# Kernel tuning notes

Hardware: AMD Instinct MI355X
Metric: run time of the kernel (lower is better)

The kernel has to match this reference:

```python
import jax, jax.numpy as jnp
import numpy as np

B, T, E, H, V = 64, 512, 256, 512, 32000  # batch, n_step, emb_size=input_size, hidden_size, n_class


def setup_inputs() -> dict:
    key = jax.random.key(0)
    ks = jax.random.split(key, 32)
    stdv = 1.0 / np.sqrt(H)  # init_weights: uniform(-1/sqrt(hidden), +1/sqrt(hidden)) on ALL params
    u = lambda k, shape: jax.random.uniform(k, shape, jnp.float32, -stdv, stdv)
    X = jax.random.randint(ks[0], (B, T), 0, V, dtype=jnp.int64)
    inp = {
        "X": X,
        "emb": u(ks[1], (V, E)),
        # layer 0 gates (U_c/V_c/b_c, V_o, b_o are dead in forward -> omitted)
        "U_f": u(ks[2], (E, H)), "V_f": u(ks[3], (H, H)), "b_f": u(ks[4], (H,)),
        "U_i": u(ks[5], (E, H)), "V_i": u(ks[6], (H, H)), "b_i": u(ks[7], (H,)),
        "U_g": u(ks[8], (E, H)), "V_g": u(ks[9], (H, H)), "b_g": u(ks[10], (H,)),
        "U_o": u(ks[11], (E, H)),
        # layer 1 gates (U_c1/V_c1/b_c1 dead -> omitted)
        "U_f1": u(ks[12], (H, H)), "V_f1": u(ks[13], (H, H)), "b_f1": u(ks[14], (H,)),
        "U_i1": u(ks[15], (H, H)), "V_i1": u(ks[16], (H, H)), "b_i1": u(ks[17], (H,)),
        "U_g1": u(ks[18], (H, H)), "V_g1": u(ks[19], (H, H)), "b_g1": u(ks[20], (H,)),
        "U_o1": u(ks[21], (H, H)), "V_o1": u(ks[22], (H, H)), "b_o1": u(ks[23], (H,)),
        # output head: nn.Linear(H, n_class, bias=False) -> store as [H, V]; b starts as ones then re-init uniform
        "W_out": u(ks[24], (H, V)), "b_out": u(ks[25], (V,)),
    }
    return inp


def reference(X, emb, U_f, V_f, b_f, U_i, V_i, b_i, U_g, V_g, b_g, U_o,
              U_f1, V_f1, b_f1, U_i1, V_i1, b_i1, U_g1, V_g1, b_g1,
              U_o1, V_o1, b_o1, W_out, b_out):
    x = emb[X]                      # [B, T, E]
    xs = jnp.swapaxes(x, 0, 1)      # [T, B, E] for scan over time

    def step(carry, x_t):
        h, c, h1, c1 = carry
        # layer 0 (NOTE: original code uses V_o1 and b_o1 for layer-0 output gate)
        f = jax.nn.sigmoid(x_t @ U_f + h @ V_f + b_f)
        i = jax.nn.sigmoid(x_t @ U_i + h @ V_i + b_i)
        g = jnp.tanh(x_t @ U_g + h @ V_g + b_g)
        c = f * c + i * g
        o = jax.nn.sigmoid(x_t @ U_o + h @ V_o1 + b_o1)
        h = o * jnp.tanh(c)
        # layer 1
        f1 = jax.nn.sigmoid(h @ U_f1 + h1 @ V_f1 + b_f1)
        i1 = jax.nn.sigmoid(h @ U_i1 + h1 @ V_i1 + b_i1)
        g1 = jnp.tanh(h @ U_g1 + h1 @ V_g1 + b_g1)
        c1 = f1 * c1 + i1 * g1
        o1 = jax.nn.sigmoid(h @ U_o1 + h1 @ V_o1 + b_o1)
        h1 = o1 * jnp.tanh(c1)
        return (h, c, h1, c1), None

    ones = jnp.ones((B, H), jnp.float32)  # original inits states to ONES
    (h, c, h1, c1), _ = jax.lax.scan(step, (ones, ones, ones, ones), xs)
    # original: model = self.U(outputs) + self.U(outputs) + self.b  (U applied twice, V unused)
    proj = h1 @ W_out
    return proj + proj + b_out      # [B, V]
```

## Files before the change

kernel.cpp:

```cpp
#include <hip/hip_runtime.h>
#include <hip/hip_bf16.h>

typedef __attribute__((ext_vector_type(8))) short bf16x8;
typedef __attribute__((ext_vector_type(4))) float f32x4;
typedef __attribute__((ext_vector_type(2))) int int32x2;

constexpr int kB = 64;
constexpr int kT = 512;
constexpr int kE = 256;
constexpr int kH = 512;
constexpr int kV = 32000;
constexpr int kBH = kB * kH;
constexpr int FSTR = 16;

static __device__ __forceinline__ unsigned short f2bf(float x) {
  __hip_bfloat16 h = __float2bfloat16(x);
  return __builtin_bit_cast(unsigned short, h);
}

static __device__ __forceinline__ f32x4 mfma16(bf16x8 a, bf16x8 b, f32x4 c) {
  return __builtin_amdgcn_mfma_f32_16x16x32_bf16(a, b, c, 0, 0, 0);
}

static __device__ __forceinline__ void issue16_sc1(const unsigned short* p, bf16x8* a) {
  asm volatile(
      "global_load_dwordx4 %0, %16, off sc1\n\t"
      "global_load_dwordx4 %1, %16, off offset:64 sc1\n\t"
      "global_load_dwordx4 %2, %16, off offset:128 sc1\n\t"
      "global_load_dwordx4 %3, %16, off offset:192 sc1\n\t"
      "global_load_dwordx4 %4, %16, off offset:256 sc1\n\t"
      "global_load_dwordx4 %5, %16, off offset:320 sc1\n\t"
      "global_load_dwordx4 %6, %16, off offset:384 sc1\n\t"
      "global_load_dwordx4 %7, %16, off offset:448 sc1\n\t"
      "global_load_dwordx4 %8, %16, off offset:512 sc1\n\t"
      "global_load_dwordx4 %9, %16, off offset:576 sc1\n\t"
      "global_load_dwordx4 %10, %16, off offset:640 sc1\n\t"
      "global_load_dwordx4 %11, %16, off offset:704 sc1\n\t"
      "global_load_dwordx4 %12, %16, off offset:768 sc1\n\t"
      "global_load_dwordx4 %13, %16, off offset:832 sc1\n\t"
      "global_load_dwordx4 %14, %16, off offset:896 sc1\n\t"
      "global_load_dwordx4 %15, %16, off offset:960 sc1"
      : "=&v"(a[0]), "=&v"(a[1]), "=&v"(a[2]), "=&v"(a[3]),
        "=&v"(a[4]), "=&v"(a[5]), "=&v"(a[6]), "=&v"(a[7]),
        "=&v"(a[8]), "=&v"(a[9]), "=&v"(a[10]), "=&v"(a[11]),
        "=&v"(a[12]), "=&v"(a[13]), "=&v"(a[14]), "=&v"(a[15])
      : "v"(p));
}

static __device__ __forceinline__ void wait_frags16(bf16x8* a) {
  asm volatile("s_waitcnt vmcnt(0)"
               : "+v"(a[0]), "+v"(a[1]), "+v"(a[2]), "+v"(a[3]),
                 "+v"(a[4]), "+v"(a[5]), "+v"(a[6]), "+v"(a[7]),
                 "+v"(a[8]), "+v"(a[9]), "+v"(a[10]), "+v"(a[11]),
                 "+v"(a[12]), "+v"(a[13]), "+v"(a[14]), "+v"(a[15])
               :
               : "memory");
}

static __device__ __forceinline__ void store_dwordx2_sc1(unsigned short* p, int32x2 v) {
  asm volatile("global_store_dwordx2 %0, %1, off sc1" ::"v"(p), "v"(v) : "memory");
}

static __device__ __forceinline__ void store_int_sc1(int* p, int v) {
  asm volatile("global_store_dword %0, %1, off sc1" ::"v"(p), "v"(v) : "memory");
}

static __device__ __forceinline__ void pollgate(const int* p, int thr) {
  while (true) {
    int v;
    asm volatile("global_load_dword %0, %1, off sc1\n\ts_waitcnt vmcnt(0)"
                 : "=&v"(v)
                 : "v"(p)
                 : "memory");
    if (__all(v >= thr)) break;
  }
}

__global__ void pack_w(const float* __restrict__ s0, const float* __restrict__ s1,
                       const float* __restrict__ s2, const float* __restrict__ s3,
                       unsigned short* __restrict__ dst, int K) {
  int o = blockIdx.x * 256 + threadIdx.x;
  if (o >= K * 2048) return;
  int j = o & 7;
  int lane = (o >> 3) & 63;
  int gate = (o >> 9) & 3;
  int r2 = o >> 11;
  int kc = r2 % (K / 32);
  int hb = r2 / (K / 32);
  int k = kc * 32 + (lane >> 4) * 8 + j;
  int hid = hb * 16 + (lane & 15);
  const float* s = (gate == 0) ? s0 : (gate == 1) ? s1 : (gate == 2) ? s2 : s3;
  dst[o] = f2bf(s[(size_t)k * kH + hid]);
}

__global__ void gather_x(const int* __restrict__ X, const float* __restrict__ emb,
                         unsigned short* __restrict__ xseq) {
  int o = blockIdx.x * 256 + threadIdx.x;
  if (o >= kT * kB * (kE / 8)) return;
  int e8 = o & 31;
  int b = (o >> 5) & 63;
  int t = o >> 11;
  int tok = X[b * kT + t];
  const float* src = emb + (size_t)tok * kE + e8 * 8;
  unsigned short tmp[8];
#pragma unroll
  for (int j = 0; j < 8; ++j) tmp[j] = f2bf(src[j]);
  unsigned short* dst = xseq + ((size_t)t * kB + b) * kE + e8 * 8;
#pragma unroll
  for (int j = 0; j < 8; ++j) dst[j] = tmp[j];
}

__global__ void init_state(unsigned short* hbuf, unsigned short* h1buf,
                           float* bcat0, float* bcat1, int* fl0, int* fl1,
                           const float* b_f, const float* b_i, const float* b_g,
                           const float* b_o1,
                           const float* b_f1, const float* b_i1, const float* b_g1) {
  int i = blockIdx.x * 256 + threadIdx.x;
  if (i < 8 * kBH) hbuf[i] = 0x3F80u;
  if (i < 2 * kBH) h1buf[i] = 0x3F80u;
  if (i < 512) {
    bcat0[i] = b_f[i];  bcat0[512 + i] = b_i[i];
    bcat0[1024 + i] = b_g[i];  bcat0[1536 + i] = b_o1[i];
    bcat1[i] = b_f1[i]; bcat1[512 + i] = b_i1[i];
    bcat1[1024 + i] = b_g1[i]; bcat1[1536 + i] = b_o1[i];
  }
  if (i < 4 * 32 * FSTR) { fl0[i] = 0; fl1[i] = 0; }
}

__global__ void __launch_bounds__(64, 1)
lstm_rec(const unsigned short* __restrict__ xseq,
         const unsigned short* __restrict__ U0p, const unsigned short* __restrict__ V0p,
         const unsigned short* __restrict__ U1p, const unsigned short* __restrict__ V1p,
         const float* __restrict__ bcat0, const float* __restrict__ bcat1,
         unsigned short* __restrict__ hbuf,
         unsigned short* __restrict__ h1buf,
         float* __restrict__ h1f,
         int* __restrict__ fl0,
         int* __restrict__ fl1)
{
  extern __shared__ unsigned short lds[];
  const int lane = threadIdx.x;
  const int wg = blockIdx.x;
  const bool isL1 = wg >= 128;
  const int wl = wg & 127;
  const int hb = wl >> 2, bt = wl & 3;
  const int l15 = lane & 15, g4 = lane >> 4;
  const int batch = bt * 16 + l15;
  const int hid4 = hb * 16 + g4 * 4;
  const int KU = isL1 ? 512 : 256;

  {
    const unsigned short* Wu = isL1 ? U1p : U0p;
    const unsigned short* Wv = isL1 ? V1p : V0p;
    const int nu = KU * 64, nv = 512 * 64;
    const bf16x8* su = (const bf16x8*)(Wu + (size_t)hb * nu);
    bf16x8* d = (bf16x8*)lds;
    for (int i = lane; i < nu / 8; i += 64) d[i] = su[i];
    const bf16x8* sv = (const bf16x8*)(Wv + (size_t)hb * nv);
    bf16x8* d2 = (bf16x8*)(lds + nu);
    for (int i = lane; i < nv / 8; i += 64) d2[i] = sv[i];
  }

  const int* pollp = (lane < 32) ? (fl0 + bt * 32 * FSTR + lane * FSTR)
                                 : (fl1 + bt * 32 * FSTR + (lane - 32) * FSTR);
  const int throff = isL1 ? (lane < 32 ? -1 : 0) : (lane < 32 ? 0 : 7);
  int* myflag = (isL1 ? fl1 : fl0) + bt * 32 * FSTR + hb * FSTR;

  const float* bc = isL1 ? bcat1 : bcat0;
  const float4 bF = *(const float4*)(bc + 0 * 512 + hid4);
  const float4 bI = *(const float4*)(bc + 1 * 512 + hid4);
  const float4 bG = *(const float4*)(bc + 2 * 512 + hid4);
  const float4 bO = *(const float4*)(bc + 3 * 512 + hid4);
  float cst[4] = {1.f, 1.f, 1.f, 1.f};

#define GATE_EPILOGUE(hv)                                                      \
  float hv[4];                                                                 \
  {                                                                            \
    const float bfv[4] = {bF.x, bF.y, bF.z, bF.w};                             \
    const float biv[4] = {bI.x, bI.y, bI.z, bI.w};                             \
    const float bgv[4] = {bG.x, bG.y, bG.z, bG.w};                             \
    const float bov[4] = {bO.x, bO.y, bO.z, bO.w};                             \
    _Pragma("unroll") for (int r = 0; r < 4; ++r) {                            \
      float fg = 1.f / (1.f + __expf(-(acc[0][r] + bfv[r])));                  \
      float ig = 1.f / (1.f + __expf(-(acc[1][r] + biv[r])));                  \
      float e2 = __expf(2.f * (acc[2][r] + bgv[r]));                           \
      float gg = (e2 - 1.f) / (e2 + 1.f);                                      \
      float og = 1.f / (1.f + __expf(-(acc[3][r] + bov[r])));                  \
      float cn = fg * cst[r] + ig * gg;                                        \
      cst[r] = cn;                                                             \
      float e2c = __expf(2.f * cn);                                            \
      hv[r] = og * (e2c - 1.f) / (e2c + 1.f);                                  \
    }                                                                          \
  }

  if (!isL1) {
    bf16x8 xr[8];
    {
      const unsigned short* xp = xseq + (size_t)batch * kE + g4 * 8;
#pragma unroll
      for (int kc = 0; kc < 8; ++kc) xr[kc] = *(const bf16x8*)(xp + kc * 32);
    }
    for (int t = 0; t < kT; ++t) {
      pollgate(pollp, t - throff);
      bf16x8 vF[16];
      issue16_sc1(hbuf + (size_t)((t + 7) & 7) * kBH + batch * kH + g4 * 8, vF);
      f32x4 acc[4] = {{0, 0, 0, 0}, {0, 0, 0, 0}, {0, 0, 0, 0}, {0, 0, 0, 0}};
#pragma unroll
      for (int kc = 0; kc < 8; ++kc) {
        const unsigned short* ab = lds + kc * 2048 + lane * 8;
        acc[0] = mfma16(*(const bf16x8*)ab, xr[kc], acc[0]);
        acc[1] = mfma16(*(const bf16x8*)(ab + 512), xr[kc], acc[1]);
        acc[2] = mfma16(*(const bf16x8*)(ab + 1024), xr[kc], acc[2]);
        acc[3] = mfma16(*(const bf16x8*)(ab + 1536), xr[kc], acc[3]);
      }
      wait_frags16(vF);
#pragma unroll
      for (int kc = 0; kc < 16; ++kc) {
        const unsigned short* ab = lds + (8 + kc) * 2048 + lane * 8;
        acc[0] = mfma16(*(const bf16x8*)ab, vF[kc], acc[0]);
        acc[1] = mfma16(*(const bf16x8*)(ab + 512), vF[kc], acc[1]);
        acc[2] = mfma16(*(const bf16x8*)(ab + 1024), vF[kc], acc[2]);
        acc[3] = mfma16(*(const bf16x8*)(ab + 1536), vF[kc], acc[3]);
      }
      GATE_EPILOGUE(hv)
      unsigned int lo = (unsigned)f2bf(hv[0]) | ((unsigned)f2bf(hv[1]) << 16);
      unsigned int hi = (unsigned)f2bf(hv[2]) | ((unsigned)f2bf(hv[3]) << 16);
      int32x2 pk = {(int)lo, (int)hi};
      store_dwordx2_sc1(hbuf + (size_t)(t & 7) * kBH + batch * kH + hid4, pk);
      if (t + 1 < kT) {
        const unsigned short* xp =
            xseq + ((size_t)(t + 1) * kB + batch) * kE + g4 * 8;
#pragma unroll
        for (int kc = 0; kc < 8; ++kc) xr[kc] = *(const bf16x8*)(xp + kc * 32);
        asm volatile("s_waitcnt vmcnt(8)" ::: "memory");
      } else {
        asm volatile("s_waitcnt vmcnt(0)" ::: "memory");
      }
      if (lane == 0) store_int_sc1(myflag, t + 1);
    }
  } else {
    for (int s = 0; s < kT; ++s) {
      pollgate(pollp, s - throff);
      bf16x8 uF[16], vF[16];
      issue16_sc1(hbuf + (size_t)(s & 7) * kBH + batch * kH + g4 * 8, uF);
      issue16_sc1(h1buf + (size_t)((s + 1) & 1) * kBH + batch * kH + g4 * 8, vF);
      wait_frags16(uF);
      wait_frags16(vF);
      f32x4 acc[4] = {{0, 0, 0, 0}, {0, 0, 0, 0}, {0, 0, 0, 0}, {0, 0, 0, 0}};
#pragma unroll
      for (int kc = 0; kc < 16; ++kc) {
        const unsigned short* ab = lds + kc * 2048 + lane * 8;
        acc[0] = mfma16(*(const bf16x8*)ab, uF[kc], acc[0]);
        acc[1] = mfma16(*(const bf16x8*)(ab + 512), uF[kc], acc[1]);
        acc[2] = mfma16(*(const bf16x8*)(ab + 1024), uF[kc], acc[2]);
        acc[3] = mfma16(*(const bf16x8*)(ab + 1536), uF[kc], acc[3]);
      }
#pragma unroll
      for (int kc = 0; kc < 16; ++kc) {
        const unsigned short* ab = lds + (16 + kc) * 2048 + lane * 8;
        acc[0] = mfma16(*(const bf16x8*)ab, vF[kc], acc[0]);
        acc[1] = mfma16(*(const bf16x8*)(ab + 512), vF[kc], acc[1]);
        acc[2] = mfma16(*(const bf16x8*)(ab + 1024), vF[kc], acc[2]);
        acc[3] = mfma16(*(const bf16x8*)(ab + 1536), vF[kc], acc[3]);
      }
      GATE_EPILOGUE(hv)
      if (s == kT - 1) {
        f32x4 hq = {hv[0], hv[1], hv[2], hv[3]};
        *(f32x4*)(h1f + (size_t)batch * kH + hid4) = hq;
      } else {
        unsigned int lo = (unsigned)f2bf(hv[0]) | ((unsigned)f2bf(hv[1]) << 16);
        unsigned int hi = (unsigned)f2bf(hv[2]) | ((unsigned)f2bf(hv[3]) << 16);
        int32x2 pk = {(int)lo, (int)hi};
        store_dwordx2_sc1(h1buf + (size_t)(s & 1) * kBH + batch * kH + hid4, pk);
      }
      asm volatile("s_waitcnt vmcnt(0)" ::: "memory");
      if (lane == 0) store_int_sc1(myflag, s + 1);
    }
  }
#undef GATE_EPILOGUE
}

__global__ void head(const float* __restrict__ h1f, const float* __restrict__ Wout,
                     const float* __restrict__ bout, float* __restrict__ out) {
  extern __shared__ float hs[];
  const int v = blockIdx.x * 256 + threadIdx.x;
  const int half = blockIdx.y;
  for (int i = threadIdx.x; i < 32 * kH; i += 256) hs[i] = h1f[half * 32 * kH + i];
  __syncthreads();
  float acc[32];
#pragma unroll
  for (int r = 0; r < 32; ++r) acc[r] = 0.f;
  for (int k = 0; k < kH; k += 4) {
    float w0 = Wout[(size_t)k * kV + v];
    float w1 = Wout[(size_t)(k + 1) * kV + v];
    float w2 = Wout[(size_t)(k + 2) * kV + v];
    float w3 = Wout[(size_t)(k + 3) * kV + v];
#pragma unroll
    for (int r = 0; r < 32; ++r) {
      float4 h4 = *(const float4*)&hs[r * kH + k];
      acc[r] += h4.x * w0 + h4.y * w1 + h4.z * w2 + h4.w * w3;
    }
  }
  float bv = bout[v];
#pragma unroll
  for (int r = 0; r < 32; ++r)
    out[(size_t)(half * 32 + r) * kV + v] = 2.f * acc[r] + bv;
}

extern "C" void kernel_launch(void* const* d_in, const int* in_sizes, int n_in,
                              void* d_out, int out_size, void* d_ws, size_t ws_size,
                              hipStream_t stream) {
  const int*   X     = (const int*)d_in[0];
  const float* emb   = (const float*)d_in[1];
  const float* U_f   = (const float*)d_in[2];
  const float* V_f   = (const float*)d_in[3];
  const float* b_f   = (const float*)d_in[4];
  const float* U_i   = (const float*)d_in[5];
  const float* V_i   = (const float*)d_in[6];
  const float* b_i   = (const float*)d_in[7];
  const float* U_g   = (const float*)d_in[8];
  const float* V_g   = (const float*)d_in[9];
  const float* b_g   = (const float*)d_in[10];
  const float* U_o   = (const float*)d_in[11];
  const float* U_f1  = (const float*)d_in[12];
  const float* V_f1  = (const float*)d_in[13];
  const float* b_f1  = (const float*)d_in[14];
  const float* U_i1  = (const float*)d_in[15];
  const float* V_i1  = (const float*)d_in[16];
  const float* b_i1  = (const float*)d_in[17];
  const float* U_g1  = (const float*)d_in[18];
  const float* V_g1  = (const float*)d_in[19];
  const float* b_g1  = (const float*)d_in[20];
  const float* U_o1  = (const float*)d_in[21];
  const float* V_o1  = (const float*)d_in[22];
  const float* b_o1  = (const float*)d_in[23];
  const float* W_out = (const float*)d_in[24];
  const float* b_out = (const float*)d_in[25];

  char* ws = (char*)d_ws;
  auto alloc = [&](size_t bytes) -> char* {
    char* p = ws;
    ws += (bytes + 255) & ~(size_t)255;
    return p;
  };
  unsigned short* U0p   = (unsigned short*)alloc((size_t)kE * 2048 * 2);
  unsigned short* V0p   = (unsigned short*)alloc((size_t)kH * 2048 * 2);
  unsigned short* U1p   = (unsigned short*)alloc((size_t)kH * 2048 * 2);
  unsigned short* V1p   = (unsigned short*)alloc((size_t)kH * 2048 * 2);
  unsigned short* xseq  = (unsigned short*)alloc((size_t)kT * kB * kE * 2);
  unsigned short* hbuf  = (unsigned short*)alloc((size_t)8 * kBH * 2);
  unsigned short* h1buf = (unsigned short*)alloc((size_t)2 * kBH * 2);
  float* h1f   = (float*)alloc((size_t)kBH * 4);
  float* bcat0 = (float*)alloc(4 * 512 * 4);
  float* bcat1 = (float*)alloc(4 * 512 * 4);
  int*   fl0   = (int*)alloc(4 * 32 * FSTR * 4);
  int*   fl1   = (int*)alloc(4 * 32 * FSTR * 4);

  pack_w<<<(kE * 2048 + 255) / 256, 256, 0, stream>>>(U_f, U_i, U_g, U_o, U0p, kE);
  pack_w<<<(kH * 2048 + 255) / 256, 256, 0, stream>>>(V_f, V_i, V_g, V_o1, V0p, kH);
  pack_w<<<(kH * 2048 + 255) / 256, 256, 0, stream>>>(U_f1, U_i1, U_g1, U_o1, U1p, kH);
  pack_w<<<(kH * 2048 + 255) / 256, 256, 0, stream>>>(V_f1, V_i1, V_g1, V_o1, V1p, kH);
  gather_x<<<(kT * kB * (kE / 8) + 255) / 256, 256, 0, stream>>>(X, emb, xseq);
  init_state<<<(8 * kBH + 255) / 256, 256, 0, stream>>>(
      hbuf, h1buf, bcat0, bcat1, fl0, fl1,
      b_f, b_i, b_g, b_o1, b_f1, b_i1, b_g1);

  (void)hipFuncSetAttribute((const void*)lstm_rec,
                            hipFuncAttributeMaxDynamicSharedMemorySize, 131072);
  void* args[] = {
      (void*)&xseq, (void*)&U0p, (void*)&V0p, (void*)&U1p, (void*)&V1p,
      (void*)&bcat0, (void*)&bcat1, (void*)&hbuf, (void*)&h1buf,
      (void*)&h1f, (void*)&fl0, (void*)&fl1};
  (void)hipLaunchCooperativeKernel((const void*)lstm_rec, dim3(256), dim3(64),
                                   args, 131072, stream);

  head<<<dim3(kV / 256, 2), 256, 65536, stream>>>(h1f, W_out, b_out, (float*)d_out);
}
```

Baseline: 2.645 ms.

## Stage vmcnt waits in recurrence, merge pack kernels, widen head to 64 rows

The recurrent kernel now waits on the h-fragment loads in groups of 4 or 8 using partial vmcnt counts, so MFMAs on early chunks can start while later loads are still in flight. The four weight-pack launches are merged into one 2D-grid launch. The head kernel now handles all 64 batch rows per block with 128KB of LDS, reading W_out once instead of twice. The tradeoffs are 64 accumulators per thread in the head, which raises register pressure, and fewer head blocks (125) to spread across the device.

```diff
diff --git a/kernel.cpp b/kernel.cpp
--- a/kernel.cpp
+++ b/kernel.cpp
@@ -47,15 +47,32 @@
       : "v"(p));
 }
 
-static __device__ __forceinline__ void wait_frags16(bf16x8* a) {
-  asm volatile("s_waitcnt vmcnt(0)"
-               : "+v"(a[0]), "+v"(a[1]), "+v"(a[2]), "+v"(a[3]),
-                 "+v"(a[4]), "+v"(a[5]), "+v"(a[6]), "+v"(a[7]),
-                 "+v"(a[8]), "+v"(a[9]), "+v"(a[10]), "+v"(a[11]),
-                 "+v"(a[12]), "+v"(a[13]), "+v"(a[14]), "+v"(a[15])
-               :
-               : "memory");
-}
+#define WAIT4(NAME, CNT)                                                    \
+  static __device__ __forceinline__ void NAME(bf16x8* a) {                  \
+    asm volatile("s_waitcnt vmcnt(" #CNT ")"                                \
+                 : "+v"(a[0]), "+v"(a[1]), "+v"(a[2]), "+v"(a[3])           \
+                 :                                                          \
+                 : "memory");                                               \
+  }
+WAIT4(wait4_vm12, 12)
+WAIT4(wait4_vm8, 8)
+WAIT4(wait4_vm4, 4)
+WAIT4(wait4_vm0, 0)
+#undef WAIT4
+
+#define WAIT8(NAME, CNT)                                                    \
+  static __device__ __forceinline__ void NAME(bf16x8* a) {                  \
+    asm volatile("s_waitcnt vmcnt(" #CNT ")"                                \
+                 : "+v"(a[0]), "+v"(a[1]), "+v"(a[2]), "+v"(a[3]),          \
+                   "+v"(a[4]), "+v"(a[5]), "+v"(a[6]), "+v"(a[7])           \
+                 :                                                          \
+                 : "memory");                                               \
+  }
+WAIT8(wait8_vm24, 24)
+WAIT8(wait8_vm16, 16)
+WAIT8(wait8_vm8, 8)
+WAIT8(wait8_vm0, 0)
+#undef WAIT8
 
 static __device__ __forceinline__ void store_dwordx2_sc1(unsigned short* p, int32x2 v) {
   asm volatile("global_store_dwordx2 %0, %1, off sc1" ::"v"(p), "v"(v) : "memory");
@@ -76,9 +93,24 @@
   }
 }
 
-__global__ void pack_w(const float* __restrict__ s0, const float* __restrict__ s1,
-                       const float* __restrict__ s2, const float* __restrict__ s3,
-                       unsigned short* __restrict__ dst, int K) {
+__global__ void pack_all(const float* __restrict__ U_f, const float* __restrict__ U_i,
+                         const float* __restrict__ U_g, const float* __restrict__ U_o,
+                         const float* __restrict__ V_f, const float* __restrict__ V_i,
+                         const float* __restrict__ V_g, const float* __restrict__ V_o1,
+                         const float* __restrict__ U_f1, const float* __restrict__ U_i1,
+                         const float* __restrict__ U_g1, const float* __restrict__ U_o1,
+                         const float* __restrict__ V_f1, const float* __restrict__ V_i1,
+                         const float* __restrict__ V_g1,
+                         unsigned short* __restrict__ U0p, unsigned short* __restrict__ V0p,
+                         unsigned short* __restrict__ U1p, unsigned short* __restrict__ V1p) {
+  const int which = blockIdx.y;
+  const float *s0, *s1, *s2, *s3;
+  unsigned short* dst;
+  int K;
+  if (which == 0)      { s0 = U_f;  s1 = U_i;  s2 = U_g;  s3 = U_o;  dst = U0p; K = kE; }
+  else if (which == 1) { s0 = V_f;  s1 = V_i;  s2 = V_g;  s3 = V_o1; dst = V0p; K = kH; }
+  else if (which == 2) { s0 = U_f1; s1 = U_i1; s2 = U_g1; s3 = U_o1; dst = U1p; K = kH; }
+  else                 { s0 = V_f1; s1 = V_i1; s2 = V_g1; s3 = V_o1; dst = V1p; K = kH; }
   int o = blockIdx.x * 256 + threadIdx.x;
   if (o >= K * 2048) return;
   int j = o & 7;
@@ -173,6 +205,15 @@
   const float4 bO = *(const float4*)(bc + 3 * 512 + hid4);
   float cst[4] = {1.f, 1.f, 1.f, 1.f};
 
+#define MFMA_KC(BASE_KC, FRAG)                                               \
+  {                                                                          \
+    const unsigned short* ab = lds + (BASE_KC) * 2048 + lane * 8;            \
+    acc[0] = mfma16(*(const bf16x8*)ab, FRAG, acc[0]);                       \
+    acc[1] = mfma16(*(const bf16x8*)(ab + 512), FRAG, acc[1]);               \
+    acc[2] = mfma16(*(const bf16x8*)(ab + 1024), FRAG, acc[2]);              \
+    acc[3] = mfma16(*(const bf16x8*)(ab + 1536), FRAG, acc[3]);              \
+  }
+
 #define GATE_EPILOGUE(hv)                                                      \
   float hv[4];                                                                 \
   {                                                                            \
@@ -206,22 +247,19 @@
       issue16_sc1(hbuf + (size_t)((t + 7) & 7) * kBH + batch * kH + g4 * 8, vF);
       f32x4 acc[4] = {{0, 0, 0, 0}, {0, 0, 0, 0}, {0, 0, 0, 0}, {0, 0, 0, 0}};
 #pragma unroll
-      for (int kc = 0; kc < 8; ++kc) {
-        const unsigned short* ab = lds + kc * 2048 + lane * 8;
-        acc[0] = mfma16(*(const bf16x8*)ab, xr[kc], acc[0]);
-        acc[1] = mfma16(*(const bf16x8*)(ab + 512), xr[kc], acc[1]);
-        acc[2] = mfma16(*(const bf16x8*)(ab + 1024), xr[kc], acc[2]);
-        acc[3] = mfma16(*(const bf16x8*)(ab + 1536), xr[kc], acc[3]);
-      }
-      wait_frags16(vF);
-#pragma unroll
-      for (int kc = 0; kc < 16; ++kc) {
-        const unsigned short* ab = lds + (8 + kc) * 2048 + lane * 8;
-        acc[0] = mfma16(*(const bf16x8*)ab, vF[kc], acc[0]);
-        acc[1] = mfma16(*(const bf16x8*)(ab + 512), vF[kc], acc[1]);
-        acc[2] = mfma16(*(const bf16x8*)(ab + 1024), vF[kc], acc[2]);
-        acc[3] = mfma16(*(const bf16x8*)(ab + 1536), vF[kc], acc[3]);
-      }
+      for (int kc = 0; kc < 8; ++kc) MFMA_KC(kc, xr[kc])
+      wait4_vm12(vF);
+#pragma unroll
+      for (int kc = 0; kc < 4; ++kc) MFMA_KC(8 + kc, vF[kc])
+      wait4_vm8(vF + 4);
+#pragma unroll
+      for (int kc = 4; kc < 8; ++kc) MFMA_KC(8 + kc, vF[kc])
+      wait4_vm4(vF + 8);
+#pragma unroll
+      for (int kc = 8; kc < 12; ++kc) MFMA_KC(8 + kc, vF[kc])
+      wait4_vm0(vF + 12);
+#pragma unroll
+      for (int kc = 12; kc < 16; ++kc) MFMA_KC(8 + kc, vF[kc])
       GATE_EPILOGUE(hv)
       unsigned int lo = (unsigned)f2bf(hv[0]) | ((unsigned)f2bf(hv[1]) << 16);
       unsigned int hi = (unsigned)f2bf(hv[2]) | ((unsigned)f2bf(hv[3]) << 16);
@@ -244,25 +282,19 @@
       bf16x8 uF[16], vF[16];
       issue16_sc1(hbuf + (size_t)(s & 7) * kBH + batch * kH + g4 * 8, uF);
       issue16_sc1(h1buf + (size_t)((s + 1) & 1) * kBH + batch * kH + g4 * 8, vF);
-      wait_frags16(uF);
-      wait_frags16(vF);
       f32x4 acc[4] = {{0, 0, 0, 0}, {0, 0, 0, 0}, {0, 0, 0, 0}, {0, 0, 0, 0}};
-#pragma unroll
-      for (int kc = 0; kc < 16; ++kc) {
-        const unsigned short* ab = lds + kc * 2048 + lane * 8;
-        acc[0] = mfma16(*(const bf16x8*)ab, uF[kc], acc[0]);
-        acc[1] = mfma16(*(const bf16x8*)(ab + 512), uF[kc], acc[1]);
-        acc[2] = mfma16(*(const bf16x8*)(ab + 1024), uF[kc], acc[2]);
-        acc[3] = mfma16(*(const bf16x8*)(ab + 1536), uF[kc], acc[3]);
-      }
-#pragma unroll
-      for (int kc = 0; kc < 16; ++kc) {
-        const unsigned short* ab = lds + (16 + kc) * 2048 + lane * 8;
-        acc[0] = mfma16(*(const bf16x8*)ab, vF[kc], acc[0]);
-        acc[1] = mfma16(*(const bf16x8*)(ab + 512), vF[kc], acc[1]);
-        acc[2] = mfma16(*(const bf16x8*)(ab + 1024), vF[kc], acc[2]);
-        acc[3] = mfma16(*(const bf16x8*)(ab + 1536), vF[kc], acc[3]);
-      }
+      wait8_vm24(uF);
+#pragma unroll
+      for (int kc = 0; kc < 8; ++kc) MFMA_KC(kc, uF[kc])
+      wait8_vm16(uF + 8);
+#pragma unroll
+      for (int kc = 8; kc < 16; ++kc) MFMA_KC(kc, uF[kc])
+      wait8_vm8(vF);
+#pragma unroll
+      for (int kc = 0; kc < 8; ++kc) MFMA_KC(16 + kc, vF[kc])
+      wait8_vm0(vF + 8);
+#pragma unroll
+      for (int kc = 8; kc < 16; ++kc) MFMA_KC(16 + kc, vF[kc])
       GATE_EPILOGUE(hv)
       if (s == kT - 1) {
         f32x4 hq = {hv[0], hv[1], hv[2], hv[3]};
@@ -278,33 +310,34 @@
     }
   }
 #undef GATE_EPILOGUE
+#undef MFMA_KC
 }
 
 __global__ void head(const float* __restrict__ h1f, const float* __restrict__ Wout,
                      const float* __restrict__ bout, float* __restrict__ out) {
   extern __shared__ float hs[];
   const int v = blockIdx.x * 256 + threadIdx.x;
-  const int half = blockIdx.y;
-  for (int i = threadIdx.x; i < 32 * kH; i += 256) hs[i] = h1f[half * 32 * kH + i];
+  for (int i = threadIdx.x; i < 64 * kH / 4; i += 256)
+    ((float4*)hs)[i] = ((const float4*)h1f)[i];
   __syncthreads();
-  float acc[32];
-#pragma unroll
-  for (int r = 0; r < 32; ++r) acc[r] = 0.f;
+  float acc[64];
+#pragma unroll
+  for (int r = 0; r < 64; ++r) acc[r] = 0.f;
   for (int k = 0; k < kH; k += 4) {
     float w0 = Wout[(size_t)k * kV + v];
     float w1 = Wout[(size_t)(k + 1) * kV + v];
     float w2 = Wout[(size_t)(k + 2) * kV + v];
     float w3 = Wout[(size_t)(k + 3) * kV + v];
 #pragma unroll
-    for (int r = 0; r < 32; ++r) {
+    for (int r = 0; r < 64; ++r) {
       float4 h4 = *(const float4*)&hs[r * kH + k];
       acc[r] += h4.x * w0 + h4.y * w1 + h4.z * w2 + h4.w * w3;
     }
   }
   float bv = bout[v];
 #pragma unroll
-  for (int r = 0; r < 32; ++r)
-    out[(size_t)(half * 32 + r) * kV + v] = 2.f * acc[r] + bv;
+  for (int r = 0; r < 64; ++r)
+    out[(size_t)r * kV + v] = 2.f * acc[r] + bv;
 }
 
 extern "C" void kernel_launch(void* const* d_in, const int* in_sizes, int n_in,
@@ -353,13 +386,13 @@
   float* h1f   = (float*)alloc((size_t)kBH * 4);
   float* bcat0 = (float*)alloc(4 * 512 * 4);
   float* bcat1 = (float*)alloc(4 * 512 * 4);
-  int*   fl0   = (int*)alloc(4 * 32 * FSTR * 4);
-  int*   fl1   = (int*)alloc(4 * 32 * FSTR * 4);
-
-  pack_w<<<(kE * 2048 + 255) / 256, 256, 0, stream>>>(U_f, U_i, U_g, U_o, U0p, kE);
-  pack_w<<<(kH * 2048 + 255) / 256, 256, 0, stream>>>(V_f, V_i, V_g, V_o1, V0p, kH);
-  pack_w<<<(kH * 2048 + 255) / 256, 256, 0, stream>>>(U_f1, U_i1, U_g1, U_o1, U1p, kH);
-  pack_w<<<(kH * 2048 + 255) / 256, 256, 0, stream>>>(V_f1, V_i1, V_g1, V_o1, V1p, kH);
+  int* fl0     = (int*)alloc(4 * 32 * FSTR * 4);
+  int* fl1     = (int*)alloc(4 * 32 * FSTR * 4);
+
+  pack_all<<<dim3((kH * 2048 + 255) / 256, 4), 256, 0, stream>>>(
+      U_f, U_i, U_g, U_o, V_f, V_i, V_g, V_o1,
+      U_f1, U_i1, U_g1, U_o1, V_f1, V_i1, V_g1,
+      U0p, V0p, U1p, V1p);
   gather_x<<<(kT * kB * (kE / 8) + 255) / 256, 256, 0, stream>>>(X, emb, xseq);
   init_state<<<(8 * kBH + 255) / 256, 256, 0, stream>>>(
       hbuf, h1buf, bcat0, bcat1, fl0, fl1,
@@ -374,5 +407,8 @@
   (void)hipLaunchCooperativeKernel((const void*)lstm_rec, dim3(256), dim3(64),
                                    args, 131072, stream);
 
-  head<<<dim3(kV / 256, 2), 256, 65536, stream>>>(h1f, W_out, b_out, (float*)d_out);
-}
+  (void)hipFuncSetAttribute((const void*)head,
+                            hipFuncAttributeMaxDynamicSharedMemorySize, 131072);
+  head<<<dim3(kV / 256, 1), 256, 131072, stream>>>(h1f, W_out, b_out,
+                                                   (float*)d_out);
+}
```

Measured after the change: 2.510 ms. -5.1%, faster.
